# Optimization experiments

Hardware: AMD Instinct MI355X
Metric: run time of the kernel (lower is better)

Reference implementation:

```python
import math
import jax, jax.numpy as jnp
import numpy as np

WINDOW_SHAPE = [30, 30, 8]
DEPTH = 8
NUM_DIMS = 3
N_POINTS = 2_000_000
BATCH = 4
SPARSE_SHAPE = np.array([32, 512, 512], dtype=np.int64)  # [D, H, W]


def _right_shift_bits(b, k):
    # shift bit-array right along last axis: prepend k zeros, drop last k
    if b.shape[-1] <= k:
        return jnp.zeros_like(b)
    pad = [(0, 0)] * (b.ndim - 1) + [(k, 0)]
    return jnp.pad(b[..., :-k], pad)


def _gray2binary(gray):
    # prefix-XOR along last axis via doubling (matches torch gray2binary)
    n = gray.shape[-1]
    shift = 2 ** (math.ceil(math.log2(n)) - 1)
    while shift > 0:
        gray = jnp.logical_xor(gray, _right_shift_bits(gray, shift))
        shift //= 2
    return gray


def hilbert_encode(locs, num_dims, num_bits):
    # locs: [N, num_dims] int, each in [0, 2**num_bits)
    n = locs.shape[0]
    # bit b of gray is the (num_bits-1-b)-th bit of the coordinate (MSB first)
    shifts_ = (num_bits - 1 - jnp.arange(num_bits, dtype=locs.dtype))
    gray = ((locs[:, :, None] >> shifts_[None, None, :]) & 1).astype(bool)  # [N, D, B]
    # Skilling's transform: small fixed loop (num_bits*num_dims = 24 iters)
    for bit in range(num_bits):
        for dim in range(num_dims):
            mask = gray[:, dim, bit]  # [N]
            g0 = jnp.logical_xor(gray[:, 0, bit + 1:], mask[:, None])
            gray = gray.at[:, 0, bit + 1:].set(g0)
            to_flip = jnp.logical_and(
                jnp.logical_not(mask)[:, None],
                jnp.logical_xor(gray[:, 0, bit + 1:], gray[:, dim, bit + 1:]),
            )
            gray = gray.at[:, dim, bit + 1:].set(
                jnp.logical_xor(gray[:, dim, bit + 1:], to_flip))
            gray = gray.at[:, 0, bit + 1:].set(
                jnp.logical_xor(gray[:, 0, bit + 1:], to_flip))
    # interleave: swapaxes(1,2) then flatten -> [N, num_bits*num_dims], MSB first
    bits = jnp.transpose(gray, (0, 2, 1)).reshape(n, num_bits * num_dims)
    hb = _gray2binary(bits)
    nb = num_bits * num_dims
    weights = jnp.asarray((1 << (nb - 1 - np.arange(nb))), dtype=jnp.int32)
    code = (hb.astype(jnp.int32) * weights).sum(-1)
    return code


def setup_inputs() -> dict:
    key = jax.random.key(0)
    kb, kz, ky, kx = jax.random.split(key, 4)
    D, H, W = [int(v) for v in SPARSE_SHAPE]
    b = jax.random.randint(kb, (N_POINTS,), 0, BATCH, dtype=jnp.int32)
    z = jax.random.randint(kz, (N_POINTS,), 0, D, dtype=jnp.int32)
    y = jax.random.randint(ky, (N_POINTS,), 0, H, dtype=jnp.int32)
    x = jax.random.randint(kx, (N_POINTS,), 0, W, dtype=jnp.int32)
    coords = jnp.stack([b, z, y, x], axis=-1)  # [N, 4]: bs, z, y, x
    return {"coords": coords, "sparse_shape": SPARSE_SHAPE, "shifts": 1}


def reference(coords, sparse_shape, shifts):
    # sparse_shape is static config: [D, H, W]; reversed -> W, H, D (as in torch)
    ss = [int(v) for v in np.asarray(sparse_shape)][::-1]
    W, H, D = ss
    wx, wy, wz = WINDOW_SHAPE
    if bool(shifts):
        sx, sy, sz = math.ceil(wx / 2), math.ceil(wy / 2), math.ceil(wz / 2)
    else:
        sx = sy = sz = 0
    b = coords[:, 0]
    x = (coords[:, 3] + sx) % W
    y = (coords[:, 2] + sy) % H
    z = (coords[:, 1] + sz) % D
    locs = jnp.stack([x, y, z], axis=-1)  # [N, 3]
    code = hilbert_encode(locs, NUM_DIMS, DEPTH)
    code = code | (b.astype(code.dtype) << (DEPTH * 3))
    coords2curve = jnp.argsort(code)
    return coords2curve
```

## Files before the change

kernel.cpp:

```cpp
#include <hip/hip_runtime.h>
#include <stdint.h>


#define THREADS 512
#define SCTH 1024
#define SWAVES (SCTH / 64)
#define TILE 4096
#define TILE2 8192
#define IDX_BITS 22
#define IDX_MASK 0x3FFFFFu

__device__ __forceinline__ int tile_of(int bid, int nwg) {
  int q = nwg >> 3, r = nwg & 7;
  int x = bid & 7, k = bid >> 3;
  return x * q + (x < r ? x : r) + k;
}

__device__ __forceinline__ uint32_t hilbert_code(uint32_t x, uint32_t y, uint32_t z) {
  uint32_t X0 = x & 255u, X1 = y & 255u, X2 = z & 255u;
#pragma unroll
  for (int p = 7; p >= 0; --p) {
    uint32_t low = (1u << p) - 1u;
    uint32_t f0 = (uint32_t)-(int)((X0 >> p) & 1u);
    X0 ^= (low & f0);
    uint32_t f1 = (uint32_t)-(int)((X1 >> p) & 1u);
    uint32_t t1 = ((X0 ^ X1) & low) & ~f1;
    X0 ^= (low & f1) ^ t1;
    X1 ^= t1;
    uint32_t f2 = (uint32_t)-(int)((X2 >> p) & 1u);
    uint32_t t2 = ((X0 ^ X2) & low) & ~f2;
    X0 ^= (low & f2) ^ t2;
    X2 ^= t2;
  }
  uint32_t G = 0;
#pragma unroll
  for (int k = 0; k < 8; ++k) {
    int p = 7 - k;
    G |= ((X0 >> p) & 1u) << (23 - 3 * k);
    G |= ((X1 >> p) & 1u) << (22 - 3 * k);
    G |= ((X2 >> p) & 1u) << (21 - 3 * k);
  }
  G ^= G >> 16; G ^= G >> 8; G ^= G >> 4; G ^= G >> 2; G ^= G >> 1;
  return G & 0xFFFFFFu;
}

__global__ __launch_bounds__(THREADS) void genkeys_hist(
    const int4* __restrict__ coords, const void* __restrict__ ss,
    const int* __restrict__ shifts, uint32_t* __restrict__ keys0,
    int* __restrict__ hist, int N) {
  __shared__ int lh[512];
  int t = threadIdx.x, b = tile_of(blockIdx.x, gridDim.x);
  lh[t] = 0;

  const int* p32 = (const int*)ss;
  int D, H, W;
  if (p32[1] == 0) { const long long* p64 = (const long long*)ss;
    D = (int)p64[0]; H = (int)p64[1]; W = (int)p64[2]; }
  else { D = p32[0]; H = p32[1]; W = p32[2]; }
  int sflag = shifts[0];
  int sx = sflag ? 15 : 0, sy = sflag ? 15 : 0, sz = sflag ? 4 : 0;
  bool wp2 = (W & (W - 1)) == 0, hp2 = (H & (H - 1)) == 0, dp2 = (D & (D - 1)) == 0;
  __syncthreads();

#pragma unroll
  for (int r = 0; r < TILE / THREADS; ++r) {
    int idx = b * TILE + r * THREADS + t;
    if (idx < N) {
      int4 c = coords[idx];
      uint32_t bb = (uint32_t)c.x;
      int zz = c.y + sz, yy = c.z + sy, xx = c.w + sx;
      uint32_t z = (uint32_t)(dp2 ? (zz & (D - 1)) : (zz % D));
      uint32_t y = (uint32_t)(hp2 ? (yy & (H - 1)) : (yy % H));
      uint32_t x = (uint32_t)(wp2 ? (xx & (W - 1)) : (xx % W));
      uint32_t code = hilbert_code(x, y, z) | (bb << 24);
      keys0[idx] = code;
      atomicAdd(&lh[code & 511u], 1);
    }
  }
  __syncthreads();
  hist[(size_t)b * 512 + t] = lh[t];
}

template <int SHIFT, int NB, int TB>
__global__ __launch_bounds__(THREADS) void hist_kernel(
    const uint32_t* __restrict__ keys, int* __restrict__ hist, int N) {
  __shared__ int lh[NB];
  int t = threadIdx.x, b = tile_of(blockIdx.x, gridDim.x);
  if (t < NB) lh[t] = 0;
  __syncthreads();
#pragma unroll
  for (int r = 0; r < TB / THREADS / 4; ++r) {
    int base = b * TB + (r * THREADS + t) * 4;
    if (base + 3 < N) {
      uint4 k = *(const uint4*)(keys + base);
      atomicAdd(&lh[(k.x >> SHIFT) & (NB - 1)], 1);
      atomicAdd(&lh[(k.y >> SHIFT) & (NB - 1)], 1);
      atomicAdd(&lh[(k.z >> SHIFT) & (NB - 1)], 1);
      atomicAdd(&lh[(k.w >> SHIFT) & (NB - 1)], 1);
    } else {
      for (int u = 0; u < 4; ++u)
        if (base + u < N) atomicAdd(&lh[(keys[base + u] >> SHIFT) & (NB - 1)], 1);
    }
  }
  __syncthreads();
  if (t < NB) hist[(size_t)b * NB + t] = lh[t];
}

__global__ __launch_bounds__(512) void scan_blocks(
    int* __restrict__ hist, int* __restrict__ digitTotals, int nblocks, int nbins) {
  __shared__ int wsum[8];
  int d = blockIdx.x, t = threadIdx.x, wave = t >> 6, lane = t & 63;
  int carry = 0;
  for (int start = 0; start < nblocks; start += 512) {
    int i = start + t;
    int vv = (i < nblocks) ? hist[(size_t)i * nbins + d] : 0;
    int x = vv;
#pragma unroll
    for (int off = 1; off < 64; off <<= 1) {
      int n = __shfl_up(x, off);
      if (lane >= off) x += n;
    }
    if (lane == 63) wsum[wave] = x;
    __syncthreads();
    int pre = 0;
    for (int w = 0; w < wave; ++w) pre += wsum[w];
    if (i < nblocks) hist[(size_t)i * nbins + d] = carry + pre + x - vv;
    int tot = 0;
    for (int w = 0; w < 8; ++w) tot += wsum[w];
    __syncthreads();
    carry += tot;
  }
  if (t == 0) digitTotals[d] = carry;
}

template <int MODE>
__global__ __launch_bounds__(SCTH) void scatter_kernel(
    const uint32_t* __restrict__ in0, const uint32_t* __restrict__ in1,
    uint32_t* __restrict__ out0, uint32_t* __restrict__ out1,
    const int* __restrict__ hist, const int* __restrict__ digitTotals, int N) {
  constexpr int NB = (MODE == 2) ? 256 : 512;
  constexpr int RB = (MODE == 2) ? 8 : 9;
  constexpr int SHIFT = (MODE == 0) ? 0 : (MODE == 1) ? 9 : 22;
  constexpr int TB = (MODE == 2) ? TILE2 : TILE;
  constexpr int RNDS = TB / SCTH;
  constexpr int CH = TB / SWAVES;
  __shared__ uint64_t sbuf[TB <= 4096 ? TB : TB / 2];
  __shared__ __align__(16) unsigned short cnt[SWAVES][NB];
  int t = threadIdx.x, b = tile_of(blockIdx.x, gridDim.x);
  int wave = t >> 6, lane = t & 63;

  int histv = 0, dt = 0;
  if (t < NB) {
    histv = hist[(size_t)b * NB + t];
    dt = digitTotals[t];
  }
  for (int i = t; i < SWAVES * NB; i += SCTH) ((unsigned short*)cnt)[i] = 0;
  __syncthreads();

  uint32_t kR[RNDS];
  uint32_t vR[(MODE == 1) ? RNDS : 1];
  int drR[RNDS];
  uint64_t ltm = (1ull << lane) - 1ull;
  int chunk0 = b * TB + wave * CH;

#pragma unroll
  for (int r = 0; r < RNDS; ++r) {
    int idx = chunk0 + r * 64 + lane;
    bool valid = idx < N;
    kR[r] = valid ? in0[idx] : 0u;
    if (MODE == 1) vR[r] = valid ? in1[idx] : 0u;
  }

#pragma unroll
  for (int r = 0; r < RNDS; ++r) {
    int idx = chunk0 + r * 64 + lane;
    bool valid = idx < N;
    int digit = (int)((kR[r] >> SHIFT) & (NB - 1));
    uint64_t eq = __ballot(valid);
#pragma unroll
    for (int bit = 0; bit < RB; ++bit) {
      uint64_t m = __ballot((digit >> bit) & 1);
      eq &= ((digit >> bit) & 1) ? m : ~m;
    }
    int waveRank = __popcll(eq & ltm);
    int cntW = __popcll(eq);
    int prior = cnt[wave][digit];
    drR[r] = valid ? (digit | ((prior + waveRank) << RB)) : -1;
    if (valid && waveRank == 0) cnt[wave][digit] = (unsigned short)(prior + cntW);
  }
  __syncthreads();

  int2* wt = (int2*)sbuf;
  int tot = 0, adjv = 0;
  int2 v = make_int2(0, 0);
  if (t < NB) {
#pragma unroll
    for (int w = 0; w < SWAVES; ++w) tot += cnt[w][t];
    v = make_int2(tot, dt);
#pragma unroll
    for (int off = 1; off < 64; off <<= 1) {
      int nx = __shfl_up(v.x, off), ny = __shfl_up(v.y, off);
      if (lane >= off) { v.x += nx; v.y += ny; }
    }
    if (lane == 63) wt[wave] = v;
  }
  __syncthreads();
  if (t < NB) {
    int2 pre = make_int2(0, 0);
    for (int w = 0; w < wave; ++w) { pre.x += wt[w].x; pre.y += wt[w].y; }
    int ds = pre.x + v.x - tot;
    adjv = histv + (pre.y + v.y - dt) - ds;
    int run = ds;
#pragma unroll
    for (int w = 0; w < SWAVES; ++w) {
      int x = cnt[w][t];
      cnt[w][t] = (unsigned short)run;
      run += x;
    }
  }
  __syncthreads();

#pragma unroll
  for (int r = 0; r < RNDS; ++r) {
    int dr = drR[r];
    if (dr >= 0) {
      int digit = dr & (NB - 1);
      int rnk = dr >> RB;
      int slot = (int)cnt[wave][digit] + rnk;
      if (MODE == 0) {
        uint32_t idxv = (uint32_t)(chunk0 + r * 64 + lane);
        sbuf[slot] = ((uint64_t)idxv << 32) | kR[r];
      } else if (MODE == 1) {
        sbuf[slot] = ((uint64_t)vR[r] << 32) | kR[r];
      } else {
        ((uint32_t*)sbuf)[slot] = kR[r];
      }
    }
  }
  __syncthreads();

  int* adjArr = (int*)cnt;
  if (t < NB) adjArr[t] = adjv;
  __syncthreads();

  int validCount = min(TB, N - b * TB);
#pragma unroll
  for (int j = 0; j < RNDS; ++j) {
    int i = j * SCTH + t;
    if (i < validCount) {
      if (MODE == 0) {
        uint64_t kv = sbuf[i];
        uint32_t key = (uint32_t)kv;
        int pos = adjArr[key & 511u] + i;
        out0[pos] = key;
        out1[pos] = (uint32_t)(kv >> 32);
      } else if (MODE == 1) {
        uint64_t kv = sbuf[i];
        uint32_t key = (uint32_t)kv, idxv = (uint32_t)(kv >> 32);
        int pos = adjArr[(key >> 9) & 511u] + i;
        out0[pos] = ((key >> 18) << IDX_BITS) | idxv;
      } else {
        uint32_t p = ((uint32_t*)sbuf)[i];
        int pos = adjArr[(p >> IDX_BITS) & 255u] + i;
        out0[pos] = p & IDX_MASK;
      }
    }
  }
}

extern "C" void kernel_launch(void* const* d_in, const int* in_sizes, int n_in,
                              void* d_out, int out_size, void* d_ws, size_t ws_size,
                              hipStream_t stream) {
  const int4* coords = (const int4*)d_in[0];
  const void* ss = d_in[1];
  const int* shifts = (const int*)d_in[2];
  int N = in_sizes[0] / 4;
  int nblocks = (N + TILE - 1) / TILE;
  int nblocks2 = (N + TILE2 - 1) / TILE2;

  char* ws = (char*)d_ws;
  size_t off = 0;
  auto alloc = [&](size_t bytes) -> void* {
    void* p = ws + off;
    off += (bytes + 255) & ~(size_t)255;
    return p;
  };
  uint32_t* keys0 = (uint32_t*)alloc((size_t)N * 4);
  uint32_t* keys1 = (uint32_t*)alloc((size_t)N * 4);
  uint32_t* vals1 = (uint32_t*)alloc((size_t)N * 4);
  uint32_t* packd = (uint32_t*)alloc((size_t)N * 4);
  int*      hist  = (int*)alloc((size_t)512 * nblocks * 4);
  int*      digitTotals = (int*)alloc(512 * 4);

  genkeys_hist<<<nblocks, THREADS, 0, stream>>>(coords, ss, shifts, keys0, hist, N);
  scan_blocks<<<512, 512, 0, stream>>>(hist, digitTotals, nblocks, 512);
  scatter_kernel<0><<<nblocks, SCTH, 0, stream>>>(
      keys0, nullptr, keys1, vals1, hist, digitTotals, N);

  hist_kernel<9, 512, TILE><<<nblocks, THREADS, 0, stream>>>(keys1, hist, N);
  scan_blocks<<<512, 512, 0, stream>>>(hist, digitTotals, nblocks, 512);
  scatter_kernel<1><<<nblocks, SCTH, 0, stream>>>(
      keys1, vals1, packd, nullptr, hist, digitTotals, N);

  hist_kernel<22, 256, TILE2><<<nblocks2, THREADS, 0, stream>>>(packd, hist, N);
  scan_blocks<<<256, 512, 0, stream>>>(hist, digitTotals, nblocks2, 256);
  scatter_kernel<2><<<nblocks2, SCTH, 0, stream>>>(
      packd, nullptr, (uint32_t*)d_out, nullptr, hist, digitTotals, N);
}
```

Before: 79.12 us.

## Fuse per-digit histogram scans into histogram kernels via last-block ticket

Removes the separate scan_blocks launches by having the last-arriving blocks of each histogram kernel take a ticket, wait for all blocks to finish, then each scan four digit columns. This eliminates three kernel launches and their gaps at the cost of a memset, a spin-wait, and an assumption that the block count is at most 512 rows per column scan.

Measured after the change: 205.9 us. +160.3%, slower.

```diff
diff --git a/kernel.cpp b/kernel.cpp
--- a/kernel.cpp
+++ b/kernel.cpp
@@ -44,11 +44,64 @@
   return G & 0xFFFFFFu;
 }
 
+__device__ __forceinline__ void scan_col(int* __restrict__ hist, int* __restrict__ dt,
+                                         int nrows, int nbins, int d, int t,
+                                         int* wsum) {
+  __syncthreads();
+  int wave = t >> 6, lane = t & 63;
+  int vv = (t < nrows) ? hist[(size_t)t * nbins + d] : 0;
+  int x = vv;
+#pragma unroll
+  for (int off = 1; off < 64; off <<= 1) {
+    int n = __shfl_up(x, off);
+    if (lane >= off) x += n;
+  }
+  if (lane == 63) wsum[wave] = x;
+  __syncthreads();
+  int pre = 0;
+  for (int w = 0; w < wave; ++w) pre += wsum[w];
+  if (t < nrows) hist[(size_t)t * nbins + d] = pre + x - vv;
+  if (t == 0) {
+    int tot = 0;
+    for (int w = 0; w < 8; ++w) tot += wsum[w];
+    dt[d] = tot;
+  }
+}
+
+template <int NBINS>
+__device__ __forceinline__ void ticket_and_scan(
+    int* __restrict__ hist, int* __restrict__ dt, int* __restrict__ done,
+    int t, int* wsum, int* sh_ticket) {
+  constexpr int NSCAN = NBINS / 4;
+  int nbG = gridDim.x;
+  __syncthreads();
+  if (t == 0) {
+    __threadfence();
+    *sh_ticket = atomicAdd(done, 1);
+  }
+  __syncthreads();
+  int ticket = *sh_ticket;
+  if (ticket >= nbG - NSCAN) {
+    if (t == 0) {
+      while (__hip_atomic_load(done, __ATOMIC_RELAXED, __HIP_MEMORY_SCOPE_AGENT) < nbG)
+        __builtin_amdgcn_s_sleep(2);
+    }
+    __syncthreads();
+    __threadfence();
+    int rank = ticket - (nbG - NSCAN);
+#pragma unroll
+    for (int c = 0; c < 4; ++c)
+      scan_col(hist, dt, nbG, NBINS, rank * 4 + c, t, wsum);
+  }
+}
+
 __global__ __launch_bounds__(THREADS) void genkeys_hist(
     const int4* __restrict__ coords, const void* __restrict__ ss,
     const int* __restrict__ shifts, uint32_t* __restrict__ keys0,
-    int* __restrict__ hist, int N) {
+    int* __restrict__ hist, int* __restrict__ dt, int* __restrict__ done, int N) {
   __shared__ int lh[512];
+  __shared__ int wsum[8];
+  __shared__ int sh_ticket;
   int t = threadIdx.x, b = tile_of(blockIdx.x, gridDim.x);
   lh[t] = 0;
 
@@ -79,12 +132,16 @@
   }
   __syncthreads();
   hist[(size_t)b * 512 + t] = lh[t];
+  ticket_and_scan<512>(hist, dt, done, t, wsum, &sh_ticket);
 }
 
 template <int SHIFT, int NB, int TB>
 __global__ __launch_bounds__(THREADS) void hist_kernel(
-    const uint32_t* __restrict__ keys, int* __restrict__ hist, int N) {
+    const uint32_t* __restrict__ keys, int* __restrict__ hist,
+    int* __restrict__ dt, int* __restrict__ done, int N) {
   __shared__ int lh[NB];
+  __shared__ int wsum[8];
+  __shared__ int sh_ticket;
   int t = threadIdx.x, b = tile_of(blockIdx.x, gridDim.x);
   if (t < NB) lh[t] = 0;
   __syncthreads();
@@ -104,33 +161,7 @@
   }
   __syncthreads();
   if (t < NB) hist[(size_t)b * NB + t] = lh[t];
-}
-
-__global__ __launch_bounds__(512) void scan_blocks(
-    int* __restrict__ hist, int* __restrict__ digitTotals, int nblocks, int nbins) {
-  __shared__ int wsum[8];
-  int d = blockIdx.x, t = threadIdx.x, wave = t >> 6, lane = t & 63;
-  int carry = 0;
-  for (int start = 0; start < nblocks; start += 512) {
-    int i = start + t;
-    int vv = (i < nblocks) ? hist[(size_t)i * nbins + d] : 0;
-    int x = vv;
-#pragma unroll
-    for (int off = 1; off < 64; off <<= 1) {
-      int n = __shfl_up(x, off);
-      if (lane >= off) x += n;
-    }
-    if (lane == 63) wsum[wave] = x;
-    __syncthreads();
-    int pre = 0;
-    for (int w = 0; w < wave; ++w) pre += wsum[w];
-    if (i < nblocks) hist[(size_t)i * nbins + d] = carry + pre + x - vv;
-    int tot = 0;
-    for (int w = 0; w < 8; ++w) tot += wsum[w];
-    __syncthreads();
-    carry += tot;
-  }
-  if (t == 0) digitTotals[d] = carry;
+  ticket_and_scan<NB>(hist, dt, done, t, wsum, &sh_ticket);
 }
 
 template <int MODE>
@@ -290,20 +321,23 @@
   uint32_t* vals1 = (uint32_t*)alloc((size_t)N * 4);
   uint32_t* packd = (uint32_t*)alloc((size_t)N * 4);
   int*      hist  = (int*)alloc((size_t)512 * nblocks * 4);
-  int*      digitTotals = (int*)alloc(512 * 4);
-
-  genkeys_hist<<<nblocks, THREADS, 0, stream>>>(coords, ss, shifts, keys0, hist, N);
-  scan_blocks<<<512, 512, 0, stream>>>(hist, digitTotals, nblocks, 512);
+  int*      dt    = (int*)alloc(512 * 4);
+  int*      done  = (int*)alloc(256);
+
+  hipMemsetAsync(done, 0, 256, stream);
+
+  genkeys_hist<<<nblocks, THREADS, 0, stream>>>(coords, ss, shifts, keys0,
+                                                hist, dt, done + 0, N);
   scatter_kernel<0><<<nblocks, SCTH, 0, stream>>>(
-      keys0, nullptr, keys1, vals1, hist, digitTotals, N);
-
-  hist_kernel<9, 512, TILE><<<nblocks, THREADS, 0, stream>>>(keys1, hist, N);
-  scan_blocks<<<512, 512, 0, stream>>>(hist, digitTotals, nblocks, 512);
+      keys0, nullptr, keys1, vals1, hist, dt, N);
+
+  hist_kernel<9, 512, TILE><<<nblocks, THREADS, 0, stream>>>(keys1, hist, dt,
+                                                             done + 1, N);
   scatter_kernel<1><<<nblocks, SCTH, 0, stream>>>(
-      keys1, vals1, packd, nullptr, hist, digitTotals, N);
-
-  hist_kernel<22, 256, TILE2><<<nblocks2, THREADS, 0, stream>>>(packd, hist, N);
-  scan_blocks<<<256, 512, 0, stream>>>(hist, digitTotals, nblocks2, 256);
+      keys1, vals1, packd, nullptr, hist, dt, N);
+
+  hist_kernel<22, 256, TILE2><<<nblocks2, THREADS, 0, stream>>>(packd, hist, dt,
+                                                                done + 2, N);
   scatter_kernel<2><<<nblocks2, SCTH, 0, stream>>>(
-      packd, nullptr, (uint32_t*)d_out, nullptr, hist, digitTotals, N);
-}
+      packd, nullptr, (uint32_t*)d_out, nullptr, hist, dt, N);
+}
```
